# Kernel tuning notes

Hardware: AMD Instinct MI355X
Metric: run time of the kernel (lower is better)

## Reference

```python
import jax, jax.numpy as jnp
import numpy as np

NUM_CLASSES = 2
OVERLAP_THRESHOLD = 0.35
NEG_POS_RATIO = 7
VARIANCES = (0.1, 0.2)
B, P, G = 16, 131072, 32


def point_form(pri):
    # center form (cx,cy,w,h) -> corner form (x1,y1,x2,y2)
    return jnp.concatenate([pri[:, :2] - pri[:, 2:] / 2,
                            pri[:, :2] + pri[:, 2:] / 2], axis=1)


def jaccard(box_a, box_b):
    # box_a [G,4], box_b [P,4], corner form -> IoU [G,P]
    max_xy = jnp.minimum(box_a[:, None, 2:], box_b[None, :, 2:])
    min_xy = jnp.maximum(box_a[:, None, :2], box_b[None, :, :2])
    inter = jnp.prod(jnp.clip(max_xy - min_xy, 0.0, None), axis=2)
    area_a = jnp.prod(box_a[:, 2:] - box_a[:, :2], axis=1)[:, None]
    area_b = jnp.prod(box_b[:, 2:] - box_b[:, :2], axis=1)[None, :]
    return inter / (area_a + area_b - inter)


def encode(matched, pri, variances):
    g_cxcy = ((matched[:, :2] + matched[:, 2:]) / 2 - pri[:, :2]) / (variances[0] * pri[:, 2:])
    g_wh = jnp.log((matched[:, 2:] - matched[:, :2]) / pri[:, 2:]) / variances[1]
    return jnp.concatenate([g_cxcy, g_wh], axis=1)


def encode_landm(matched, pri, variances):
    m = matched.reshape(-1, 5, 2)  # [P,5,2]
    g = (m - pri[:, None, :2]) / (variances[0] * pri[:, None, 2:])
    return g.reshape(-1, 10)


def match_one(truths, landms, labels, pri):
    overlaps = jaccard(truths, point_form(pri))          # [G,P]
    best_prior_idx = jnp.argmax(overlaps, axis=1)        # [G] best prior per gt
    best_truth_overlap = jnp.max(overlaps, axis=0)       # [P]
    best_truth_idx = jnp.argmax(overlaps, axis=0)        # [P]
    # ensure each gt keeps its best prior
    best_truth_overlap = best_truth_overlap.at[best_prior_idx].set(2.0)
    best_truth_idx = best_truth_idx.at[best_prior_idx].set(jnp.arange(truths.shape[0]))
    matches = truths[best_truth_idx]                     # [P,4]
    conf = jnp.where(best_truth_overlap < OVERLAP_THRESHOLD, 0, labels[best_truth_idx])
    loc = encode(matches, pri, VARIANCES)
    landm = encode_landm(landms[best_truth_idx], pri, VARIANCES)
    return loc, conf, landm


def smooth_l1(pred, gt):
    d = jnp.abs(pred - gt)
    return jnp.where(d < 1.0, 0.5 * d * d, d - 0.5)


def multibox_loss(conf_data, loc_data, landm_data, priors, targets):
    batch_size, num_priors = loc_data.shape[0], priors.shape[0]
    truths = targets[:, :, :4]
    landms = targets[:, :, 4:14]
    labels = targets[:, :, 14].astype(jnp.int32)
    loc_t, conf_t, landm_t = jax.vmap(lambda t, l, lb: match_one(t, l, lb, priors))(truths, landms, labels)

    pos = conf_t > 0                                      # [B,P]
    num_pos_total = jnp.maximum(pos.sum().astype(loc_data.dtype), 1.0)
    num_pos_per_image = pos.sum(axis=1, keepdims=True)    # [B,1]
    posf = pos.astype(loc_data.dtype)

    loss_box = (smooth_l1(loc_data, loc_t).sum(-1) * posf).sum()
    loss_landm = (smooth_l1(landm_data, landm_t).sum(-1) * posf).sum()

    logp = jax.nn.log_softmax(conf_data, axis=-1)         # [B,P,C]
    ce = -jnp.take_along_axis(logp, jnp.clip(conf_t, 0, None)[..., None], axis=-1)[..., 0]
    loss_c = jnp.where(pos | (conf_t < 0), 0.0, ce)       # zero pos & ignored
    # hard negative mining: rank by descending loss via double argsort
    loss_idx = jnp.argsort(-loss_c, axis=1)
    idx_rank = jnp.argsort(loss_idx, axis=1)
    num_neg = jnp.minimum(NEG_POS_RATIO * num_pos_per_image, num_priors - 1)
    neg = idx_rank < num_neg
    pn = (pos | neg).astype(conf_data.dtype)
    loss_c_final = (ce * pn).sum()
    return (loss_box / num_pos_total, loss_c_final / num_pos_total, loss_landm / num_pos_total)


def setup_inputs() -> dict:
    key = jax.random.key(0)
    k1, k2, k3, k4, k5, k6, k7 = jax.random.split(key, 7)
    conf_data = jax.random.normal(k1, (B, P, NUM_CLASSES), dtype=jnp.float32)
    loc_data = jax.random.normal(k2, (B, P, 4), dtype=jnp.float32)
    landm_data = jax.random.normal(k3, (B, P, 10), dtype=jnp.float32)
    # priors in center form
    pc = jax.random.uniform(k4, (P, 2), minval=0.0, maxval=1.0)
    pwh = jax.random.uniform(k5, (P, 2), minval=0.02, maxval=0.3)
    priors = jnp.concatenate([pc, pwh], axis=1).astype(jnp.float32)
    # targets: [B,G,15] = corner box(4) + landms(10) + label(1)
    c = jax.random.uniform(k6, (B, G, 2), minval=0.2, maxval=0.8)
    s = jax.random.uniform(k7, (B, G, 2), minval=0.05, maxval=0.3)
    box = jnp.concatenate([c - s / 2, c + s / 2], axis=-1)
    lm = jax.random.uniform(jax.random.fold_in(key, 99), (B, G, 10), minval=0.0, maxval=1.0)
    lbl = jnp.ones((B, G, 1), dtype=jnp.float32)
    targets = jnp.concatenate([box, lm, lbl], axis=-1).astype(jnp.float32)
    return {"conf_data": conf_data, "loc_data": loc_data, "landm_data": landm_data,
            "priors": priors, "targets": targets}


def reference(conf_data, loc_data, landm_data, priors, targets):
    return multibox_loss(conf_data, loc_data, landm_data, priors, targets)
```

## Files before the change

### kernel.cpp

```cpp
#include <hip/hip_runtime.h>
#include <math.h>

#define B_ 16
#define P_ 131072
#define G_ 32
constexpr float OVER_THR = 0.35f;
constexpr float VAR0 = 0.1f;
constexpr float VAR1 = 0.2f;
constexpr int NEG_POS = 7;
constexpr int UNR = 8;
constexpr int LOSS_X = P_ / 256;
constexpr int LOSS_BLOCKS = LOSS_X * B_;
constexpr int NBIN13 = 8192;
constexpr int NBIN8 = 256;
constexpr int NBIN11 = 2048;
constexpr int SCAN_BLKS = 16;

__device__ inline float s1(float d) {
    d = fabsf(d);
    return d < 1.f ? 0.5f * d * d : d - 0.5f;
}

__device__ inline unsigned long long shfl_xor_u64(unsigned long long x, int m) {
    unsigned lo = (unsigned)x, hi = (unsigned)(x >> 32);
    lo = __shfl_xor(lo, m);
    hi = __shfl_xor(hi, m);
    return ((unsigned long long)hi << 32) | lo;
}

template <int NB>
__device__ void topk_select(const unsigned* __restrict__ h, unsigned rem,
                            int* out_bin, unsigned* out_rem) {
    constexpr int CHUNK = NB / 256;
    const int tid = threadIdx.x;
    unsigned cnt[CHUNK];
    unsigned csum = 0;
#pragma unroll
    for (int j = 0; j < CHUNK; ++j) { cnt[j] = h[tid * CHUNK + j]; csum += cnt[j]; }
    __shared__ unsigned ss[256];
    ss[tid] = csum;
    __syncthreads();
    for (int off = 1; off < 256; off <<= 1) {
        unsigned other = (tid + off < 256) ? ss[tid + off] : 0u;
        __syncthreads();
        ss[tid] += other;
        __syncthreads();
    }
    unsigned incl = ss[tid];
    unsigned excl = incl - csum;
    if (excl < rem && incl >= rem) {
        unsigned r = rem - excl, cum = 0;
        int selbin = tid * CHUNK;
#pragma unroll
        for (int j = CHUNK - 1; j >= 0; --j) {
            unsigned c = cnt[j];
            if (cum + c >= r) { selbin = tid * CHUNK + j; r = r - cum; break; }
            cum += c;
        }
        *out_bin = selbin;
        *out_rem = r;
    }
}

__global__ __launch_bounds__(256, 3) void k_match(
        const float4* __restrict__ priors4, const float* __restrict__ targets,
        float* __restrict__ bt_ov, unsigned char* __restrict__ bt_idx,
        unsigned long long* __restrict__ pack) {
    const int b = blockIdx.y;
    const int base = blockIdx.x * (256 * UNR);
    const int tid = threadIdx.x;
    __shared__ float tb[G_][5];
    __shared__ unsigned long long red[G_][4];
    if (tid < G_ * 4) {
        int g = tid >> 2, j = tid & 3;
        tb[g][j] = targets[((size_t)b * G_ + g) * 15 + j];
    }
    __syncthreads();
    if (tid < G_) tb[tid][4] = (tb[tid][2] - tb[tid][0]) * (tb[tid][3] - tb[tid][1]);
    __syncthreads();

    float px1[UNR], py1[UNR], px2[UNR], py2[UNR], pap[UNR], best[UNR];
    int bidx[UNR];
#pragma unroll
    for (int j = 0; j < UNR; ++j) {
        float4 pr = priors4[base + j * 256 + tid];
        px1[j] = pr.x - pr.z * 0.5f;  py1[j] = pr.y - pr.w * 0.5f;
        px2[j] = pr.x + pr.z * 0.5f;  py2[j] = pr.y + pr.w * 0.5f;
        pap[j] = pr.z * pr.w;
        best[j] = -1.0f; bidx[j] = 0;
    }
    const int lane = tid & 63, wave = tid >> 6;
#pragma unroll 2
    for (int g = 0; g < G_; ++g) {
        float t0 = tb[g][0], t1 = tb[g][1], t2 = tb[g][2], t3 = tb[g][3], ta = tb[g][4];
        unsigned long long pk = 0ull;
#pragma unroll
        for (int j = 0; j < UNR; ++j) {
            float iw = fminf(t2, px2[j]) - fmaxf(t0, px1[j]);
            float ih = fminf(t3, py2[j]) - fmaxf(t1, py1[j]);
            float inter = fmaxf(iw, 0.f) * fmaxf(ih, 0.f);
            float iou = inter * __builtin_amdgcn_rcpf(ta + pap[j] - inter);
            if (iou > best[j]) { best[j] = iou; bidx[j] = g; }
            unsigned p = (unsigned)(base + j * 256 + tid);
            unsigned long long cand =
                ((unsigned long long)__float_as_uint(iou) << 32) | (unsigned)(~p);
            if (cand > pk) pk = cand;
        }
#pragma unroll
        for (int off = 32; off > 0; off >>= 1) {
            unsigned long long o = shfl_xor_u64(pk, off);
            if (o > pk) pk = o;
        }
        if (lane == 0) red[g][wave] = pk;
    }
    __syncthreads();
    if (tid < G_) {
        unsigned long long m = red[tid][0];
#pragma unroll
        for (int w = 1; w < 4; ++w) if (red[tid][w] > m) m = red[tid][w];
        atomicMax(&pack[b * G_ + tid], m);
    }
#pragma unroll
    for (int j = 0; j < UNR; ++j) {
        int p = base + j * 256 + tid;
        size_t o = (size_t)b * P_ + p;
        bt_ov[o] = best[j];
        bt_idx[o] = (unsigned char)bidx[j];
    }
}

__global__ void k_override(const unsigned long long* __restrict__ pack,
                           float* __restrict__ bt_ov, unsigned char* __restrict__ bt_idx) {
    int b = threadIdx.x;
    if (b >= B_) return;
    for (int g = 0; g < G_; ++g) {
        unsigned long long pk = pack[b * G_ + g];
        unsigned p = ~(unsigned)(pk & 0xFFFFFFFFull);
        if (p < P_) {
            bt_ov[(size_t)b * P_ + p] = 2.0f;
            bt_idx[(size_t)b * P_ + p] = (unsigned char)g;
        }
    }
}

__global__ __launch_bounds__(256) void k_loss(
        const float2* __restrict__ conf2, const float4* __restrict__ loc4,
        const float* __restrict__ landm, const float4* __restrict__ priors4,
        const float* __restrict__ targets,
        const float* __restrict__ bt_ov, const unsigned char* __restrict__ bt_idx,
        float* __restrict__ ce_neg,
        double* __restrict__ pb, double* __restrict__ pl,
        double* __restrict__ pc, int* __restrict__ pn) {
    const int b = blockIdx.y;
    const int p = blockIdx.x * 256 + threadIdx.x;
    const int tid = threadIdx.x;
    __shared__ float tg[G_ * 15];
    for (int i = tid; i < G_ * 15; i += 256) tg[i] = targets[(size_t)b * G_ * 15 + i];
    __syncthreads();

    const size_t gp = (size_t)b * P_ + p;
    float ov = bt_ov[gp];
    int ti = bt_idx[gp];
    const float* t = &tg[ti * 15];
    float label = t[14];
    int conf_t = (ov < OVER_THR) ? 0 : (int)label;
    bool pos = conf_t > 0;
    int cls = conf_t > 0 ? conf_t : 0;

    float2 c2 = conf2[gp];
    float mx = fmaxf(c2.x, c2.y);
    float lse = mx + logf(expf(c2.x - mx) + expf(c2.y - mx));
    float ce = lse - (cls ? c2.y : c2.x);
    ce_neg[gp] = (!pos && conf_t >= 0) ? ce : 0.f;

    float lb = 0.f, ll = 0.f;
    if (pos) {
        float4 pr = priors4[p];
        float vx = VAR0 * pr.z, vy = VAR0 * pr.w;
        float g0 = ((t[0] + t[2]) * 0.5f - pr.x) / vx;
        float g1 = ((t[1] + t[3]) * 0.5f - pr.y) / vy;
        float g2 = logf((t[2] - t[0]) / pr.z) / VAR1;
        float g3 = logf((t[3] - t[1]) / pr.w) / VAR1;
        float4 ld = loc4[gp];
        lb = s1(ld.x - g0) + s1(ld.y - g1) + s1(ld.z - g2) + s1(ld.w - g3);
        const float* lmp = landm + gp * 10;
#pragma unroll
        for (int i = 0; i < 5; ++i) {
            float2 lm = *(const float2*)(lmp + 2 * i);
            ll += s1(lm.x - (t[4 + 2 * i] - pr.x) / vx)
                + s1(lm.y - (t[5 + 2 * i] - pr.y) / vy);
        }
    }
    double vb = lb, vl = ll, vc = pos ? (double)ce : 0.0;
    int vp = pos ? 1 : 0;
#pragma unroll
    for (int off = 32; off > 0; off >>= 1) {
        vb += __shfl_xor(vb, off);
        vl += __shfl_xor(vl, off);
        vc += __shfl_xor(vc, off);
        vp += __shfl_xor(vp, off);
    }
    __shared__ double rb[4], rl[4], rc[4];
    __shared__ int rp[4];
    int lane = tid & 63, wave = tid >> 6;
    if (lane == 0) { rb[wave] = vb; rl[wave] = vl; rc[wave] = vc; rp[wave] = vp; }
    __syncthreads();
    if (tid == 0) {
        double sb = 0, sl = 0, sc = 0; int sp = 0;
        for (int w = 0; w < 4; ++w) { sb += rb[w]; sl += rl[w]; sc += rc[w]; sp += rp[w]; }
        int bi = blockIdx.y * LOSS_X + blockIdx.x;
        pb[bi] = sb; pl[bi] = sl; pc[bi] = sc; pn[bi] = sp;
    }
}

__global__ __launch_bounds__(1024) void k_hist13(
        const float* __restrict__ ce_neg, unsigned* __restrict__ hist) {
    const int b = blockIdx.y;
    const int tid = threadIdx.x;
    __shared__ unsigned h[NBIN13];
    for (int i = tid; i < NBIN13; i += 1024) h[i] = 0;
    __syncthreads();
    const float4* v4 = (const float4*)(ce_neg + (size_t)b * P_);
    const int c4 = P_ / SCAN_BLKS / 4;
    const int s4 = blockIdx.x * c4;
    for (int i = s4 + tid; i < s4 + c4; i += 1024) {
        float4 x = v4[i];
        atomicAdd(&h[__float_as_uint(x.x) >> 19], 1u);
        atomicAdd(&h[__float_as_uint(x.y) >> 19], 1u);
        atomicAdd(&h[__float_as_uint(x.z) >> 19], 1u);
        atomicAdd(&h[__float_as_uint(x.w) >> 19], 1u);
    }
    __syncthreads();
    unsigned* gh = hist + b * NBIN13;
    for (int i = tid; i < NBIN13; i += 1024)
        if (h[i]) atomicAdd(&gh[i], h[i]);
}

__global__ __launch_bounds__(256) void k_sel13(
        const unsigned* __restrict__ hist, const int* __restrict__ pn,
        int* __restrict__ sel, int* __restrict__ remk, int* __restrict__ npos) {
    const int b = blockIdx.x;
    const int tid = threadIdx.x;
    __shared__ int s_np;
    __shared__ int rnp[4];
    int loc = 0;
    for (int i = tid; i < LOSS_X; i += 256) loc += pn[b * LOSS_X + i];
#pragma unroll
    for (int off = 32; off > 0; off >>= 1) loc += __shfl_xor(loc, off);
    int lane = tid & 63, wave = tid >> 6;
    if (lane == 0) rnp[wave] = loc;
    __syncthreads();
    if (tid == 0) { int s = rnp[0] + rnp[1] + rnp[2] + rnp[3]; s_np = s; npos[b] = s; }
    __syncthreads();
    long long k = (long long)NEG_POS * s_np;
    if (k > P_ - 1) k = P_ - 1;
    if (k <= 0) { if (tid == 0) sel[b] = -1; return; }

    __shared__ int s_bin;
    __shared__ unsigned s_rem;
    topk_select<NBIN13>(hist + b * NBIN13, (unsigned)k, &s_bin, &s_rem);
    __syncthreads();
    if (tid == 0) { sel[b] = s_bin; remk[b] = (int)s_rem; }
}

__global__ __launch_bounds__(1024) void k_hist8(
        const float* __restrict__ ce_neg, const int* __restrict__ sel,
        unsigned* __restrict__ hist8) {
    const int b = blockIdx.y;
    const int s13 = sel[b];
    if (s13 < 0) return;
    const int tid = threadIdx.x;
    __shared__ unsigned h[NBIN8];
    if (tid < NBIN8) h[tid] = 0;
    __syncthreads();
    const float4* v4 = (const float4*)(ce_neg + (size_t)b * P_);
    const int c4 = P_ / SCAN_BLKS / 4;
    const int s4 = blockIdx.x * c4;
    for (int i = s4 + tid; i < s4 + c4; i += 1024) {
        float4 x = v4[i];
        unsigned u0 = __float_as_uint(x.x), u1 = __float_as_uint(x.y);
        unsigned u2 = __float_as_uint(x.z), u3 = __float_as_uint(x.w);
        if ((int)(u0 >> 19) == s13) atomicAdd(&h[(u0 >> 11) & 255u], 1u);
        if ((int)(u1 >> 19) == s13) atomicAdd(&h[(u1 >> 11) & 255u], 1u);
        if ((int)(u2 >> 19) == s13) atomicAdd(&h[(u2 >> 11) & 255u], 1u);
        if ((int)(u3 >> 19) == s13) atomicAdd(&h[(u3 >> 11) & 255u], 1u);
    }
    __syncthreads();
    if (tid < NBIN8 && h[tid]) atomicAdd(&hist8[b * NBIN8 + tid], h[tid]);
}

__global__ __launch_bounds__(256) void k_sel8(
        const unsigned* __restrict__ hist8, const int* __restrict__ sel,
        unsigned* __restrict__ pref, int* __restrict__ remk) {
    const int b = blockIdx.x;
    if (sel[b] < 0) return;
    __shared__ int s_bin;
    __shared__ unsigned s_rem;
    topk_select<NBIN8>(hist8 + b * NBIN8, (unsigned)remk[b], &s_bin, &s_rem);
    __syncthreads();
    if (threadIdx.x == 0) {
        pref[b] = ((unsigned)sel[b] << 8) | (unsigned)s_bin;
        remk[b] = (int)s_rem;
    }
}

__global__ __launch_bounds__(1024) void k_hist11(
        const float* __restrict__ ce_neg, const int* __restrict__ sel,
        const unsigned* __restrict__ pref, unsigned* __restrict__ hist11) {
    const int b = blockIdx.y;
    if (sel[b] < 0) return;
    const unsigned pf = pref[b];
    const int tid = threadIdx.x;
    __shared__ unsigned h[NBIN11];
    for (int i = tid; i < NBIN11; i += 1024) h[i] = 0;
    __syncthreads();
    const float4* v4 = (const float4*)(ce_neg + (size_t)b * P_);
    const int c4 = P_ / SCAN_BLKS / 4;
    const int s4 = blockIdx.x * c4;
    for (int i = s4 + tid; i < s4 + c4; i += 1024) {
        float4 x = v4[i];
        unsigned u0 = __float_as_uint(x.x), u1 = __float_as_uint(x.y);
        unsigned u2 = __float_as_uint(x.z), u3 = __float_as_uint(x.w);
        if ((u0 >> 11) == pf) atomicAdd(&h[u0 & 2047u], 1u);
        if ((u1 >> 11) == pf) atomicAdd(&h[u1 & 2047u], 1u);
        if ((u2 >> 11) == pf) atomicAdd(&h[u2 & 2047u], 1u);
        if ((u3 >> 11) == pf) atomicAdd(&h[u3 & 2047u], 1u);
    }
    __syncthreads();
    unsigned* gh = hist11 + b * NBIN11;
    for (int i = tid; i < NBIN11; i += 1024)
        if (h[i]) atomicAdd(&gh[i], h[i]);
}

__global__ __launch_bounds__(256) void k_sel11(
        const unsigned* __restrict__ hist11, const int* __restrict__ sel,
        const unsigned* __restrict__ pref, const int* __restrict__ remk,
        unsigned* __restrict__ thr, double* __restrict__ tot) {
    const int b = blockIdx.x;
    if (sel[b] < 0) { if (threadIdx.x == 0) thr[b] = 0xFFFFFFFFu; return; }
    __shared__ int s_bin;
    __shared__ unsigned s_rem;
    topk_select<NBIN11>(hist11 + b * NBIN11, (unsigned)remk[b], &s_bin, &s_rem);
    __syncthreads();
    if (threadIdx.x == 0) {
        unsigned t = (pref[b] << 11) | (unsigned)s_bin;
        thr[b] = t;
        atomicAdd(&tot[2], (double)s_rem * (double)__uint_as_float(t));
    }
}

__global__ __launch_bounds__(1024) void k_sumtop(
        const float* __restrict__ ce_neg, const unsigned* __restrict__ thr,
        double* __restrict__ tot) {
    const int b = blockIdx.y;
    const unsigned t = thr[b];
    if (t == 0xFFFFFFFFu) return;
    const int tid = threadIdx.x;
    const float4* v4 = (const float4*)(ce_neg + (size_t)b * P_);
    const int c4 = P_ / SCAN_BLKS / 4;
    const int s4 = blockIdx.x * c4;
    double loc = 0;
    for (int i = s4 + tid; i < s4 + c4; i += 1024) {
        float4 x = v4[i];
        if (__float_as_uint(x.x) > t) loc += x.x;
        if (__float_as_uint(x.y) > t) loc += x.y;
        if (__float_as_uint(x.z) > t) loc += x.z;
        if (__float_as_uint(x.w) > t) loc += x.w;
    }
#pragma unroll
    for (int off = 32; off > 0; off >>= 1) loc += __shfl_xor(loc, off);
    __shared__ double rs[16];
    int lane = tid & 63, wave = tid >> 6;
    if (lane == 0) rs[wave] = loc;
    __syncthreads();
    if (tid == 0) {
        double s = 0;
        for (int w = 0; w < 16; ++w) s += rs[w];
        atomicAdd(&tot[2], s);
    }
}

__global__ __launch_bounds__(1024) void k_final(
        const double* __restrict__ pb, const double* __restrict__ pl,
        const double* __restrict__ pc, const int* __restrict__ npos,
        const double* __restrict__ tot, float* __restrict__ out) {
    int tid = threadIdx.x;
    double sb = 0, sl = 0, sc = 0;
    for (int i = tid; i < LOSS_BLOCKS; i += 1024) {
        sb += pb[i]; sl += pl[i]; sc += pc[i];
    }
#pragma unroll
    for (int off = 32; off > 0; off >>= 1) {
        sb += __shfl_xor(sb, off);
        sl += __shfl_xor(sl, off);
        sc += __shfl_xor(sc, off);
    }
    __shared__ double rb[16], rl[16], rc[16];
    int lane = tid & 63, wave = tid >> 6;
    if (lane == 0) { rb[wave] = sb; rl[wave] = sl; rc[wave] = sc; }
    __syncthreads();
    if (tid == 0) {
        double b2 = 0, l2 = 0, c2 = 0;
        for (int w = 0; w < 16; ++w) { b2 += rb[w]; l2 += rl[w]; c2 += rc[w]; }
        long long tp = 0;
        for (int b = 0; b < B_; ++b) tp += npos[b];
        double n = tp > 0 ? (double)tp : 1.0;
        out[0] = (float)(b2 / n);
        out[1] = (float)((c2 + tot[2]) / n);
        out[2] = (float)(l2 / n);
    }
}

extern "C" void kernel_launch(void* const* d_in, const int* in_sizes, int n_in,
                              void* d_out, int out_size, void* d_ws, size_t ws_size,
                              hipStream_t stream) {
    const float* conf    = (const float*)d_in[0];
    const float* loc     = (const float*)d_in[1];
    const float* landm   = (const float*)d_in[2];
    const float* priors  = (const float*)d_in[3];
    const float* targets = (const float*)d_in[4];

    char* ws = (char*)d_ws;
    double* tot = (double*)ws;
    int* npos = (int*)(ws + 64);
    int* sel  = (int*)(ws + 128);
    int* remk = (int*)(ws + 192);
    unsigned* pref = (unsigned*)(ws + 256);
    unsigned* thr  = (unsigned*)(ws + 320);
    unsigned long long* pack = (unsigned long long*)(ws + 512);
    unsigned* hist13 = (unsigned*)(ws + 4608);
    unsigned* hist8  = hist13 + (size_t)B_ * NBIN13;
    unsigned* hist11 = hist8 + (size_t)B_ * NBIN8;
    size_t zero_bytes = 4608 + (size_t)B_ * (NBIN13 + NBIN8 + NBIN11) * 4;
    size_t big = (zero_bytes + 255) & ~(size_t)255;
    size_t BP = (size_t)B_ * P_;
    float* bt_ov = (float*)(ws + big);
    unsigned char* bt_idx = (unsigned char*)(ws + big + BP * 4);
    float* ce_neg = (float*)(ws + big + BP * 5);
    char* part = ws + big + BP * 9;
    double* pb = (double*)part;
    double* pl = (double*)(part + LOSS_BLOCKS * 8);
    double* pc = (double*)(part + LOSS_BLOCKS * 16);
    int*    pn = (int*)(part + LOSS_BLOCKS * 24);

    hipMemsetAsync(ws, 0, zero_bytes, stream);
    k_match<<<dim3(P_ / (256 * UNR), B_), 256, 0, stream>>>(
        (const float4*)priors, targets, bt_ov, bt_idx, pack);
    k_override<<<1, 64, 0, stream>>>(pack, bt_ov, bt_idx);
    k_loss<<<dim3(LOSS_X, B_), 256, 0, stream>>>(
        (const float2*)conf, (const float4*)loc, landm, (const float4*)priors,
        targets, bt_ov, bt_idx, ce_neg, pb, pl, pc, pn);
    k_hist13<<<dim3(SCAN_BLKS, B_), 1024, 0, stream>>>(ce_neg, hist13);
    k_sel13<<<B_, 256, 0, stream>>>(hist13, pn, sel, remk, npos);
    k_hist8<<<dim3(SCAN_BLKS, B_), 1024, 0, stream>>>(ce_neg, sel, hist8);
    k_sel8<<<B_, 256, 0, stream>>>(hist8, sel, pref, remk);
    k_hist11<<<dim3(SCAN_BLKS, B_), 1024, 0, stream>>>(ce_neg, sel, pref, hist11);
    k_sel11<<<B_, 256, 0, stream>>>(hist11, sel, pref, remk, thr, tot);
    k_sumtop<<<dim3(SCAN_BLKS, B_), 1024, 0, stream>>>(ce_neg, thr, tot);
    k_final<<<1, 1024, 0, stream>>>(pb, pl, pc, npos, tot, (float*)d_out);
}
```

Before: 128.5 us.

## Fuse radix-select passes with per-bin sums and last-block selection, drop override kernel

Restructures the hard-negative top-k. Each radix pass now builds count and sum histograms together, and the last block to finish (found with an atomic ticket) does the bin selection. This cuts the 7 select/hist kernels plus the final sum-above-threshold pass down to 3 scan kernels. The best-prior override is folded into k_loss as a per-thread compare against the 32 packed indices, k_match drops to UNR=4 with an in-thread argmax plus ds_swizzle reductions, and npos is accumulated with atomics. Float atomic sums in shared and global memory make the result order-dependent and add LDS atomic traffic in every pass.

```diff
diff --git a/kernel.cpp b/kernel.cpp
--- a/kernel.cpp
+++ b/kernel.cpp
@@ -8,12 +8,12 @@
 constexpr float VAR0 = 0.1f;
 constexpr float VAR1 = 0.2f;
 constexpr int NEG_POS = 7;
-constexpr int UNR = 8;
+constexpr int UNR = 4;
 constexpr int LOSS_X = P_ / 256;
 constexpr int LOSS_BLOCKS = LOSS_X * B_;
-constexpr int NBIN13 = 8192;
-constexpr int NBIN8 = 256;
-constexpr int NBIN11 = 2048;
+constexpr int NB1 = 4096;
+constexpr int NB2 = 256;
+constexpr int NB3 = 4096;
 constexpr int SCAN_BLKS = 16;
 
 __device__ inline float s1(float d) {
@@ -28,38 +28,64 @@
     return ((unsigned long long)hi << 32) | lo;
 }
 
+template <int IMM>
+__device__ inline unsigned long long swz64(unsigned long long x) {
+    unsigned lo = (unsigned)__builtin_amdgcn_ds_swizzle((int)(unsigned)x, IMM);
+    unsigned hi = (unsigned)__builtin_amdgcn_ds_swizzle((int)(unsigned)(x >> 32), IMM);
+    return ((unsigned long long)hi << 32) | lo;
+}
+
 template <int NB>
-__device__ void topk_select(const unsigned* __restrict__ h, unsigned rem,
-                            int* out_bin, unsigned* out_rem) {
-    constexpr int CHUNK = NB / 256;
+__device__ void blk_select(const unsigned* __restrict__ gc, unsigned rem,
+                           int* sbin, unsigned* srem) {
+    constexpr int CHUNK = (NB + 1023) / 1024;
     const int tid = threadIdx.x;
     unsigned cnt[CHUNK];
     unsigned csum = 0;
 #pragma unroll
-    for (int j = 0; j < CHUNK; ++j) { cnt[j] = h[tid * CHUNK + j]; csum += cnt[j]; }
-    __shared__ unsigned ss[256];
+    for (int j = 0; j < CHUNK; ++j) {
+        int idx = tid * CHUNK + j;
+        unsigned c = (idx < NB) ? gc[idx] : 0u;
+        cnt[j] = c; csum += c;
+    }
+    __shared__ unsigned ss[1024];
     ss[tid] = csum;
     __syncthreads();
-    for (int off = 1; off < 256; off <<= 1) {
-        unsigned other = (tid + off < 256) ? ss[tid + off] : 0u;
+    for (int off = 1; off < 1024; off <<= 1) {
+        unsigned o = (tid + off < 1024) ? ss[tid + off] : 0u;
         __syncthreads();
-        ss[tid] += other;
+        ss[tid] += o;
         __syncthreads();
     }
-    unsigned incl = ss[tid];
-    unsigned excl = incl - csum;
+    unsigned incl = ss[tid], excl = incl - csum;
     if (excl < rem && incl >= rem) {
         unsigned r = rem - excl, cum = 0;
-        int selbin = tid * CHUNK;
+        int sb_ = tid * CHUNK;
 #pragma unroll
         for (int j = CHUNK - 1; j >= 0; --j) {
             unsigned c = cnt[j];
-            if (cum + c >= r) { selbin = tid * CHUNK + j; r = r - cum; break; }
+            if (cum + c >= r) { sb_ = tid * CHUNK + j; r -= cum; break; }
             cum += c;
         }
-        *out_bin = selbin;
-        *out_rem = r;
-    }
+        *sbin = sb_; *srem = r;
+    }
+    __syncthreads();
+}
+
+template <int NB>
+__device__ double blk_sum_above(const float* __restrict__ gs, int bin) {
+    const int tid = threadIdx.x;
+    double a = 0;
+    for (int i = bin + 1 + tid; i < NB; i += 1024) a += (double)gs[i];
+#pragma unroll
+    for (int off = 32; off > 0; off >>= 1) a += __shfl_xor(a, off);
+    __shared__ double rs[16];
+    int lane = tid & 63, wave = tid >> 6;
+    if (lane == 0) rs[wave] = a;
+    __syncthreads();
+    double t = 0;
+    if (tid == 0) for (int w = 0; w < 16; ++w) t += rs[w];
+    return t;
 }
 
 __global__ __launch_bounds__(256, 3) void k_match(
@@ -69,14 +95,15 @@
     const int b = blockIdx.y;
     const int base = blockIdx.x * (256 * UNR);
     const int tid = threadIdx.x;
-    __shared__ float tb[G_][5];
+    __shared__ float4 tb4[G_];
+    __shared__ float tA[G_];
     __shared__ unsigned long long red[G_][4];
-    if (tid < G_ * 4) {
-        int g = tid >> 2, j = tid & 3;
-        tb[g][j] = targets[((size_t)b * G_ + g) * 15 + j];
-    }
-    __syncthreads();
-    if (tid < G_) tb[tid][4] = (tb[tid][2] - tb[tid][0]) * (tb[tid][3] - tb[tid][1]);
+    if (tid < G_) {
+        const float* tp = targets + ((size_t)b * G_ + tid) * 15;
+        float x1 = tp[0], y1 = tp[1], x2 = tp[2], y2 = tp[3];
+        tb4[tid] = make_float4(x1, y1, x2, y2);
+        tA[tid] = (x2 - x1) * (y2 - y1);
+    }
     __syncthreads();
 
     float px1[UNR], py1[UNR], px2[UNR], py2[UNR], pap[UNR], best[UNR];
@@ -92,25 +119,28 @@
     const int lane = tid & 63, wave = tid >> 6;
 #pragma unroll 2
     for (int g = 0; g < G_; ++g) {
-        float t0 = tb[g][0], t1 = tb[g][1], t2 = tb[g][2], t3 = tb[g][3], ta = tb[g][4];
-        unsigned long long pk = 0ull;
+        float4 t = tb4[g];
+        float ta = tA[g];
+        float gb = -1.0f; int gj = 0;
 #pragma unroll
         for (int j = 0; j < UNR; ++j) {
-            float iw = fminf(t2, px2[j]) - fmaxf(t0, px1[j]);
-            float ih = fminf(t3, py2[j]) - fmaxf(t1, py1[j]);
+            float iw = fminf(t.z, px2[j]) - fmaxf(t.x, px1[j]);
+            float ih = fminf(t.w, py2[j]) - fmaxf(t.y, py1[j]);
             float inter = fmaxf(iw, 0.f) * fmaxf(ih, 0.f);
             float iou = inter * __builtin_amdgcn_rcpf(ta + pap[j] - inter);
             if (iou > best[j]) { best[j] = iou; bidx[j] = g; }
-            unsigned p = (unsigned)(base + j * 256 + tid);
-            unsigned long long cand =
-                ((unsigned long long)__float_as_uint(iou) << 32) | (unsigned)(~p);
-            if (cand > pk) pk = cand;
+            if (iou > gb) { gb = iou; gj = j; }
         }
-#pragma unroll
-        for (int off = 32; off > 0; off >>= 1) {
-            unsigned long long o = shfl_xor_u64(pk, off);
-            if (o > pk) pk = o;
-        }
+        unsigned p = (unsigned)(base + (gj << 8) + tid);
+        unsigned long long pk =
+            ((unsigned long long)__float_as_uint(gb) << 32) | (unsigned)(~p);
+        unsigned long long o;
+        o = shfl_xor_u64(pk, 32);  if (o > pk) pk = o;
+        o = swz64<0x401F>(pk);     if (o > pk) pk = o;
+        o = swz64<0x201F>(pk);     if (o > pk) pk = o;
+        o = swz64<0x101F>(pk);     if (o > pk) pk = o;
+        o = swz64<0x081F>(pk);     if (o > pk) pk = o;
+        o = swz64<0x041F>(pk);     if (o > pk) pk = o;
         if (lane == 0) red[g][wave] = pk;
     }
     __syncthreads();
@@ -129,38 +159,29 @@
     }
 }
 
-__global__ void k_override(const unsigned long long* __restrict__ pack,
-                           float* __restrict__ bt_ov, unsigned char* __restrict__ bt_idx) {
-    int b = threadIdx.x;
-    if (b >= B_) return;
-    for (int g = 0; g < G_; ++g) {
-        unsigned long long pk = pack[b * G_ + g];
-        unsigned p = ~(unsigned)(pk & 0xFFFFFFFFull);
-        if (p < P_) {
-            bt_ov[(size_t)b * P_ + p] = 2.0f;
-            bt_idx[(size_t)b * P_ + p] = (unsigned char)g;
-        }
-    }
-}
-
 __global__ __launch_bounds__(256) void k_loss(
         const float2* __restrict__ conf2, const float4* __restrict__ loc4,
         const float* __restrict__ landm, const float4* __restrict__ priors4,
-        const float* __restrict__ targets,
+        const float* __restrict__ targets, const unsigned long long* __restrict__ pack,
         const float* __restrict__ bt_ov, const unsigned char* __restrict__ bt_idx,
         float* __restrict__ ce_neg,
         double* __restrict__ pb, double* __restrict__ pl,
-        double* __restrict__ pc, int* __restrict__ pn) {
+        double* __restrict__ pc, int* __restrict__ npos) {
     const int b = blockIdx.y;
     const int p = blockIdx.x * 256 + threadIdx.x;
     const int tid = threadIdx.x;
     __shared__ float tg[G_ * 15];
+    __shared__ unsigned ptg[G_];
     for (int i = tid; i < G_ * 15; i += 256) tg[i] = targets[(size_t)b * G_ * 15 + i];
+    if (tid < G_) ptg[tid] = ~(unsigned)(pack[b * G_ + tid] & 0xFFFFFFFFull);
     __syncthreads();
 
     const size_t gp = (size_t)b * P_ + p;
     float ov = bt_ov[gp];
     int ti = bt_idx[gp];
+#pragma unroll
+    for (int g = 0; g < G_; ++g)
+        if ((unsigned)p == ptg[g]) { ov = 2.0f; ti = g; }
     const float* t = &tg[ti * 15];
     float label = t[14];
     int conf_t = (ov < OVER_THR) ? 0 : (int)label;
@@ -209,69 +230,22 @@
         double sb = 0, sl = 0, sc = 0; int sp = 0;
         for (int w = 0; w < 4; ++w) { sb += rb[w]; sl += rl[w]; sc += rc[w]; sp += rp[w]; }
         int bi = blockIdx.y * LOSS_X + blockIdx.x;
-        pb[bi] = sb; pl[bi] = sl; pc[bi] = sc; pn[bi] = sp;
-    }
-}
-
-__global__ __launch_bounds__(1024) void k_hist13(
-        const float* __restrict__ ce_neg, unsigned* __restrict__ hist) {
+        pb[bi] = sb; pl[bi] = sl; pc[bi] = sc;
+        if (sp) atomicAdd(&npos[b], sp);
+    }
+}
+
+__global__ __launch_bounds__(1024) void k_ms1(
+        const float* __restrict__ ce_neg, const double* __restrict__ pb,
+        const double* __restrict__ pl, const double* __restrict__ pc,
+        const int* __restrict__ npos, unsigned* __restrict__ gcnt,
+        float* __restrict__ gsum, int* __restrict__ sel, unsigned* __restrict__ remk,
+        int* __restrict__ tick, double* __restrict__ imgsum, double* __restrict__ tot) {
     const int b = blockIdx.y;
     const int tid = threadIdx.x;
-    __shared__ unsigned h[NBIN13];
-    for (int i = tid; i < NBIN13; i += 1024) h[i] = 0;
-    __syncthreads();
-    const float4* v4 = (const float4*)(ce_neg + (size_t)b * P_);
-    const int c4 = P_ / SCAN_BLKS / 4;
-    const int s4 = blockIdx.x * c4;
-    for (int i = s4 + tid; i < s4 + c4; i += 1024) {
-        float4 x = v4[i];
-        atomicAdd(&h[__float_as_uint(x.x) >> 19], 1u);
-        atomicAdd(&h[__float_as_uint(x.y) >> 19], 1u);
-        atomicAdd(&h[__float_as_uint(x.z) >> 19], 1u);
-        atomicAdd(&h[__float_as_uint(x.w) >> 19], 1u);
-    }
-    __syncthreads();
-    unsigned* gh = hist + b * NBIN13;
-    for (int i = tid; i < NBIN13; i += 1024)
-        if (h[i]) atomicAdd(&gh[i], h[i]);
-}
-
-__global__ __launch_bounds__(256) void k_sel13(
-        const unsigned* __restrict__ hist, const int* __restrict__ pn,
-        int* __restrict__ sel, int* __restrict__ remk, int* __restrict__ npos) {
-    const int b = blockIdx.x;
-    const int tid = threadIdx.x;
-    __shared__ int s_np;
-    __shared__ int rnp[4];
-    int loc = 0;
-    for (int i = tid; i < LOSS_X; i += 256) loc += pn[b * LOSS_X + i];
-#pragma unroll
-    for (int off = 32; off > 0; off >>= 1) loc += __shfl_xor(loc, off);
-    int lane = tid & 63, wave = tid >> 6;
-    if (lane == 0) rnp[wave] = loc;
-    __syncthreads();
-    if (tid == 0) { int s = rnp[0] + rnp[1] + rnp[2] + rnp[3]; s_np = s; npos[b] = s; }
-    __syncthreads();
-    long long k = (long long)NEG_POS * s_np;
-    if (k > P_ - 1) k = P_ - 1;
-    if (k <= 0) { if (tid == 0) sel[b] = -1; return; }
-
-    __shared__ int s_bin;
-    __shared__ unsigned s_rem;
-    topk_select<NBIN13>(hist + b * NBIN13, (unsigned)k, &s_bin, &s_rem);
-    __syncthreads();
-    if (tid == 0) { sel[b] = s_bin; remk[b] = (int)s_rem; }
-}
-
-__global__ __launch_bounds__(1024) void k_hist8(
-        const float* __restrict__ ce_neg, const int* __restrict__ sel,
-        unsigned* __restrict__ hist8) {
-    const int b = blockIdx.y;
-    const int s13 = sel[b];
-    if (s13 < 0) return;
-    const int tid = threadIdx.x;
-    __shared__ unsigned h[NBIN8];
-    if (tid < NBIN8) h[tid] = 0;
+    __shared__ unsigned hc[NB1];
+    __shared__ float hs[NB1];
+    for (int i = tid; i < NB1; i += 1024) { hc[i] = 0; hs[i] = 0.f; }
     __syncthreads();
     const float4* v4 = (const float4*)(ce_neg + (size_t)b * P_);
     const int c4 = P_ / SCAN_BLKS / 4;
@@ -280,39 +254,64 @@
         float4 x = v4[i];
         unsigned u0 = __float_as_uint(x.x), u1 = __float_as_uint(x.y);
         unsigned u2 = __float_as_uint(x.z), u3 = __float_as_uint(x.w);
-        if ((int)(u0 >> 19) == s13) atomicAdd(&h[(u0 >> 11) & 255u], 1u);
-        if ((int)(u1 >> 19) == s13) atomicAdd(&h[(u1 >> 11) & 255u], 1u);
-        if ((int)(u2 >> 19) == s13) atomicAdd(&h[(u2 >> 11) & 255u], 1u);
-        if ((int)(u3 >> 19) == s13) atomicAdd(&h[(u3 >> 11) & 255u], 1u);
-    }
-    __syncthreads();
-    if (tid < NBIN8 && h[tid]) atomicAdd(&hist8[b * NBIN8 + tid], h[tid]);
-}
-
-__global__ __launch_bounds__(256) void k_sel8(
-        const unsigned* __restrict__ hist8, const int* __restrict__ sel,
-        unsigned* __restrict__ pref, int* __restrict__ remk) {
-    const int b = blockIdx.x;
-    if (sel[b] < 0) return;
-    __shared__ int s_bin;
-    __shared__ unsigned s_rem;
-    topk_select<NBIN8>(hist8 + b * NBIN8, (unsigned)remk[b], &s_bin, &s_rem);
-    __syncthreads();
-    if (threadIdx.x == 0) {
-        pref[b] = ((unsigned)sel[b] << 8) | (unsigned)s_bin;
-        remk[b] = (int)s_rem;
-    }
-}
-
-__global__ __launch_bounds__(1024) void k_hist11(
+        atomicAdd(&hc[u0 >> 20], 1u); atomicAdd(&hs[u0 >> 20], x.x);
+        atomicAdd(&hc[u1 >> 20], 1u); atomicAdd(&hs[u1 >> 20], x.y);
+        atomicAdd(&hc[u2 >> 20], 1u); atomicAdd(&hs[u2 >> 20], x.z);
+        atomicAdd(&hc[u3 >> 20], 1u); atomicAdd(&hs[u3 >> 20], x.w);
+    }
+    __syncthreads();
+    unsigned* gc = gcnt + b * NB1;
+    float* gs = gsum + b * NB1;
+    for (int i = tid; i < NB1; i += 1024)
+        if (hc[i]) { atomicAdd(&gc[i], hc[i]); atomicAdd(&gs[i], hs[i]); }
+    __threadfence();
+    __shared__ int amLast;
+    if (tid == 0) amLast = (atomicAdd(&tick[b], 1) == SCAN_BLKS - 1);
+    __syncthreads();
+    if (!amLast) return;
+    __threadfence();
+    double sb = 0, sl = 0, sc = 0;
+    for (int i = tid; i < LOSS_X; i += 1024) {
+        sb += pb[b * LOSS_X + i]; sl += pl[b * LOSS_X + i]; sc += pc[b * LOSS_X + i];
+    }
+#pragma unroll
+    for (int off = 32; off > 0; off >>= 1) {
+        sb += __shfl_xor(sb, off); sl += __shfl_xor(sl, off); sc += __shfl_xor(sc, off);
+    }
+    __shared__ double r3[16][3];
+    int lane = tid & 63, wave = tid >> 6;
+    if (lane == 0) { r3[wave][0] = sb; r3[wave][1] = sl; r3[wave][2] = sc; }
+    __syncthreads();
+    if (tid == 0) {
+        double a = 0, c = 0, d = 0;
+        for (int w = 0; w < 16; ++w) { a += r3[w][0]; c += r3[w][1]; d += r3[w][2]; }
+        imgsum[b * 3 + 0] = a; imgsum[b * 3 + 1] = c; imgsum[b * 3 + 2] = d;
+    }
+    long long k = (long long)NEG_POS * npos[b];
+    if (k > P_ - 1) k = P_ - 1;
+    if (k <= 0) { if (tid == 0) sel[b] = -1; return; }
+    __shared__ int sb_;
+    __shared__ unsigned sr_;
+    blk_select<NB1>(gc, (unsigned)k, &sb_, &sr_);
+    double above = blk_sum_above<NB1>(gs, sb_);
+    if (tid == 0) {
+        atomicAdd(&tot[2], above);
+        sel[b] = sb_; remk[b] = sr_;
+    }
+}
+
+__global__ __launch_bounds__(1024) void k_ms2(
         const float* __restrict__ ce_neg, const int* __restrict__ sel,
-        const unsigned* __restrict__ pref, unsigned* __restrict__ hist11) {
+        unsigned* __restrict__ gcnt, float* __restrict__ gsum,
+        unsigned* __restrict__ pref, unsigned* __restrict__ remk,
+        int* __restrict__ tick, double* __restrict__ tot) {
     const int b = blockIdx.y;
-    if (sel[b] < 0) return;
-    const unsigned pf = pref[b];
-    const int tid = threadIdx.x;
-    __shared__ unsigned h[NBIN11];
-    for (int i = tid; i < NBIN11; i += 1024) h[i] = 0;
+    const int s1v = sel[b];
+    if (s1v < 0) return;
+    const int tid = threadIdx.x;
+    __shared__ unsigned hc[NB2];
+    __shared__ float hs[NB2];
+    if (tid < NB2) { hc[tid] = 0; hs[tid] = 0.f; }
     __syncthreads();
     const float4* v4 = (const float4*)(ce_neg + (size_t)b * P_);
     const int c4 = P_ / SCAN_BLKS / 4;
@@ -321,93 +320,94 @@
         float4 x = v4[i];
         unsigned u0 = __float_as_uint(x.x), u1 = __float_as_uint(x.y);
         unsigned u2 = __float_as_uint(x.z), u3 = __float_as_uint(x.w);
-        if ((u0 >> 11) == pf) atomicAdd(&h[u0 & 2047u], 1u);
-        if ((u1 >> 11) == pf) atomicAdd(&h[u1 & 2047u], 1u);
-        if ((u2 >> 11) == pf) atomicAdd(&h[u2 & 2047u], 1u);
-        if ((u3 >> 11) == pf) atomicAdd(&h[u3 & 2047u], 1u);
-    }
-    __syncthreads();
-    unsigned* gh = hist11 + b * NBIN11;
-    for (int i = tid; i < NBIN11; i += 1024)
-        if (h[i]) atomicAdd(&gh[i], h[i]);
-}
-
-__global__ __launch_bounds__(256) void k_sel11(
-        const unsigned* __restrict__ hist11, const int* __restrict__ sel,
-        const unsigned* __restrict__ pref, const int* __restrict__ remk,
-        unsigned* __restrict__ thr, double* __restrict__ tot) {
-    const int b = blockIdx.x;
-    if (sel[b] < 0) { if (threadIdx.x == 0) thr[b] = 0xFFFFFFFFu; return; }
-    __shared__ int s_bin;
-    __shared__ unsigned s_rem;
-    topk_select<NBIN11>(hist11 + b * NBIN11, (unsigned)remk[b], &s_bin, &s_rem);
-    __syncthreads();
-    if (threadIdx.x == 0) {
-        unsigned t = (pref[b] << 11) | (unsigned)s_bin;
-        thr[b] = t;
-        atomicAdd(&tot[2], (double)s_rem * (double)__uint_as_float(t));
-    }
-}
-
-__global__ __launch_bounds__(1024) void k_sumtop(
-        const float* __restrict__ ce_neg, const unsigned* __restrict__ thr,
-        double* __restrict__ tot) {
+        if ((int)(u0 >> 20) == s1v) { atomicAdd(&hc[(u0 >> 12) & 255u], 1u); atomicAdd(&hs[(u0 >> 12) & 255u], x.x); }
+        if ((int)(u1 >> 20) == s1v) { atomicAdd(&hc[(u1 >> 12) & 255u], 1u); atomicAdd(&hs[(u1 >> 12) & 255u], x.y); }
+        if ((int)(u2 >> 20) == s1v) { atomicAdd(&hc[(u2 >> 12) & 255u], 1u); atomicAdd(&hs[(u2 >> 12) & 255u], x.z); }
+        if ((int)(u3 >> 20) == s1v) { atomicAdd(&hc[(u3 >> 12) & 255u], 1u); atomicAdd(&hs[(u3 >> 12) & 255u], x.w); }
+    }
+    __syncthreads();
+    unsigned* gc = gcnt + b * NB2;
+    float* gs = gsum + b * NB2;
+    if (tid < NB2 && hc[tid]) { atomicAdd(&gc[tid], hc[tid]); atomicAdd(&gs[tid], hs[tid]); }
+    __threadfence();
+    __shared__ int amLast;
+    if (tid == 0) amLast = (atomicAdd(&tick[b], 1) == SCAN_BLKS - 1);
+    __syncthreads();
+    if (!amLast) return;
+    __threadfence();
+    __shared__ int sb_;
+    __shared__ unsigned sr_;
+    blk_select<NB2>(gc, remk[b], &sb_, &sr_);
+    double above = blk_sum_above<NB2>(gs, sb_);
+    if (tid == 0) {
+        atomicAdd(&tot[2], above);
+        pref[b] = ((unsigned)s1v << 8) | (unsigned)sb_;
+        remk[b] = sr_;
+    }
+}
+
+__global__ __launch_bounds__(1024) void k_ms3(
+        const float* __restrict__ ce_neg, const int* __restrict__ sel,
+        const unsigned* __restrict__ pref, const unsigned* __restrict__ remk,
+        unsigned* __restrict__ gcnt, float* __restrict__ gsum,
+        int* __restrict__ tick, double* __restrict__ tot) {
     const int b = blockIdx.y;
-    const unsigned t = thr[b];
-    if (t == 0xFFFFFFFFu) return;
-    const int tid = threadIdx.x;
+    if (sel[b] < 0) return;
+    const unsigned pf = pref[b];
+    const int tid = threadIdx.x;
+    __shared__ unsigned hc[NB3];
+    __shared__ float hs[NB3];
+    for (int i = tid; i < NB3; i += 1024) { hc[i] = 0; hs[i] = 0.f; }
+    __syncthreads();
     const float4* v4 = (const float4*)(ce_neg + (size_t)b * P_);
     const int c4 = P_ / SCAN_BLKS / 4;
     const int s4 = blockIdx.x * c4;
-    double loc = 0;
     for (int i = s4 + tid; i < s4 + c4; i += 1024) {
         float4 x = v4[i];
-        if (__float_as_uint(x.x) > t) loc += x.x;
-        if (__float_as_uint(x.y) > t) loc += x.y;
-        if (__float_as_uint(x.z) > t) loc += x.z;
-        if (__float_as_uint(x.w) > t) loc += x.w;
-    }
-#pragma unroll
-    for (int off = 32; off > 0; off >>= 1) loc += __shfl_xor(loc, off);
-    __shared__ double rs[16];
-    int lane = tid & 63, wave = tid >> 6;
-    if (lane == 0) rs[wave] = loc;
-    __syncthreads();
+        unsigned u0 = __float_as_uint(x.x), u1 = __float_as_uint(x.y);
+        unsigned u2 = __float_as_uint(x.z), u3 = __float_as_uint(x.w);
+        if ((u0 >> 12) == pf) { atomicAdd(&hc[u0 & 4095u], 1u); atomicAdd(&hs[u0 & 4095u], x.x); }
+        if ((u1 >> 12) == pf) { atomicAdd(&hc[u1 & 4095u], 1u); atomicAdd(&hs[u1 & 4095u], x.y); }
+        if ((u2 >> 12) == pf) { atomicAdd(&hc[u2 & 4095u], 1u); atomicAdd(&hs[u2 & 4095u], x.z); }
+        if ((u3 >> 12) == pf) { atomicAdd(&hc[u3 & 4095u], 1u); atomicAdd(&hs[u3 & 4095u], x.w); }
+    }
+    __syncthreads();
+    unsigned* gc = gcnt + b * NB3;
+    float* gs = gsum + b * NB3;
+    for (int i = tid; i < NB3; i += 1024)
+        if (hc[i]) { atomicAdd(&gc[i], hc[i]); atomicAdd(&gs[i], hs[i]); }
+    __threadfence();
+    __shared__ int amLast;
+    if (tid == 0) amLast = (atomicAdd(&tick[b], 1) == SCAN_BLKS - 1);
+    __syncthreads();
+    if (!amLast) return;
+    __threadfence();
+    __shared__ int sb_;
+    __shared__ unsigned sr_;
+    blk_select<NB3>(gc, remk[b], &sb_, &sr_);
+    double above = blk_sum_above<NB3>(gs, sb_);
     if (tid == 0) {
-        double s = 0;
-        for (int w = 0; w < 16; ++w) s += rs[w];
-        atomicAdd(&tot[2], s);
-    }
-}
-
-__global__ __launch_bounds__(1024) void k_final(
-        const double* __restrict__ pb, const double* __restrict__ pl,
-        const double* __restrict__ pc, const int* __restrict__ npos,
-        const double* __restrict__ tot, float* __restrict__ out) {
-    int tid = threadIdx.x;
-    double sb = 0, sl = 0, sc = 0;
-    for (int i = tid; i < LOSS_BLOCKS; i += 1024) {
-        sb += pb[i]; sl += pl[i]; sc += pc[i];
-    }
-#pragma unroll
-    for (int off = 32; off > 0; off >>= 1) {
-        sb += __shfl_xor(sb, off);
-        sl += __shfl_xor(sl, off);
-        sc += __shfl_xor(sc, off);
-    }
-    __shared__ double rb[16], rl[16], rc[16];
-    int lane = tid & 63, wave = tid >> 6;
-    if (lane == 0) { rb[wave] = sb; rl[wave] = sl; rc[wave] = sc; }
-    __syncthreads();
-    if (tid == 0) {
-        double b2 = 0, l2 = 0, c2 = 0;
-        for (int w = 0; w < 16; ++w) { b2 += rb[w]; l2 += rl[w]; c2 += rc[w]; }
+        unsigned T = (pf << 12) | (unsigned)sb_;
+        atomicAdd(&tot[2], above + (double)sr_ * (double)__uint_as_float(T));
+    }
+}
+
+__global__ void k_final(const double* __restrict__ imgsum,
+                        const int* __restrict__ npos,
+                        const double* __restrict__ tot, float* __restrict__ out) {
+    if (threadIdx.x == 0) {
+        double sb = 0, sl = 0, sc = 0;
         long long tp = 0;
-        for (int b = 0; b < B_; ++b) tp += npos[b];
+        for (int b = 0; b < B_; ++b) {
+            sb += imgsum[b * 3 + 0];
+            sl += imgsum[b * 3 + 1];
+            sc += imgsum[b * 3 + 2];
+            tp += npos[b];
+        }
         double n = tp > 0 ? (double)tp : 1.0;
-        out[0] = (float)(b2 / n);
-        out[1] = (float)((c2 + tot[2]) / n);
-        out[2] = (float)(l2 / n);
+        out[0] = (float)(sb / n);
+        out[1] = (float)((sc + tot[2]) / n);
+        out[2] = (float)(sl / n);
     }
 }
 
@@ -424,14 +424,20 @@
     double* tot = (double*)ws;
     int* npos = (int*)(ws + 64);
     int* sel  = (int*)(ws + 128);
-    int* remk = (int*)(ws + 192);
+    unsigned* remk = (unsigned*)(ws + 192);
     unsigned* pref = (unsigned*)(ws + 256);
-    unsigned* thr  = (unsigned*)(ws + 320);
+    int* tick1 = (int*)(ws + 320);
+    int* tick2 = (int*)(ws + 384);
+    int* tick3 = (int*)(ws + 448);
     unsigned long long* pack = (unsigned long long*)(ws + 512);
-    unsigned* hist13 = (unsigned*)(ws + 4608);
-    unsigned* hist8  = hist13 + (size_t)B_ * NBIN13;
-    unsigned* hist11 = hist8 + (size_t)B_ * NBIN8;
-    size_t zero_bytes = 4608 + (size_t)B_ * (NBIN13 + NBIN8 + NBIN11) * 4;
+    double* imgsum = (double*)(ws + 4608);
+    unsigned* gcnt1 = (unsigned*)(ws + 5120);
+    float*    gsum1 = (float*)((char*)gcnt1 + (size_t)B_ * NB1 * 4);
+    unsigned* gcnt2 = (unsigned*)((char*)gsum1 + (size_t)B_ * NB1 * 4);
+    float*    gsum2 = (float*)((char*)gcnt2 + (size_t)B_ * NB2 * 4);
+    unsigned* gcnt3 = (unsigned*)((char*)gsum2 + (size_t)B_ * NB2 * 4);
+    float*    gsum3 = (float*)((char*)gcnt3 + (size_t)B_ * NB3 * 4);
+    size_t zero_bytes = 5120 + (size_t)B_ * (NB1 * 2 + NB2 * 2 + NB3 * 2) * 4;
     size_t big = (zero_bytes + 255) & ~(size_t)255;
     size_t BP = (size_t)B_ * P_;
     float* bt_ov = (float*)(ws + big);
@@ -441,21 +447,18 @@
     double* pb = (double*)part;
     double* pl = (double*)(part + LOSS_BLOCKS * 8);
     double* pc = (double*)(part + LOSS_BLOCKS * 16);
-    int*    pn = (int*)(part + LOSS_BLOCKS * 24);
 
     hipMemsetAsync(ws, 0, zero_bytes, stream);
     k_match<<<dim3(P_ / (256 * UNR), B_), 256, 0, stream>>>(
         (const float4*)priors, targets, bt_ov, bt_idx, pack);
-    k_override<<<1, 64, 0, stream>>>(pack, bt_ov, bt_idx);
     k_loss<<<dim3(LOSS_X, B_), 256, 0, stream>>>(
         (const float2*)conf, (const float4*)loc, landm, (const float4*)priors,
-        targets, bt_ov, bt_idx, ce_neg, pb, pl, pc, pn);
-    k_hist13<<<dim3(SCAN_BLKS, B_), 1024, 0, stream>>>(ce_neg, hist13);
-    k_sel13<<<B_, 256, 0, stream>>>(hist13, pn, sel, remk, npos);
-    k_hist8<<<dim3(SCAN_BLKS, B_), 1024, 0, stream>>>(ce_neg, sel, hist8);
-    k_sel8<<<B_, 256, 0, stream>>>(hist8, sel, pref, remk);
-    k_hist11<<<dim3(SCAN_BLKS, B_), 1024, 0, stream>>>(ce_neg, sel, pref, hist11);
-    k_sel11<<<B_, 256, 0, stream>>>(hist11, sel, pref, remk, thr, tot);
-    k_sumtop<<<dim3(SCAN_BLKS, B_), 1024, 0, stream>>>(ce_neg, thr, tot);
-    k_final<<<1, 1024, 0, stream>>>(pb, pl, pc, npos, tot, (float*)d_out);
-}
+        targets, pack, bt_ov, bt_idx, ce_neg, pb, pl, pc, npos);
+    k_ms1<<<dim3(SCAN_BLKS, B_), 1024, 0, stream>>>(
+        ce_neg, pb, pl, pc, npos, gcnt1, gsum1, sel, remk, tick1, imgsum, tot);
+    k_ms2<<<dim3(SCAN_BLKS, B_), 1024, 0, stream>>>(
+        ce_neg, sel, gcnt2, gsum2, pref, remk, tick2, tot);
+    k_ms3<<<dim3(SCAN_BLKS, B_), 1024, 0, stream>>>(
+        ce_neg, sel, pref, remk, gcnt3, gsum3, tick3, tot);
+    k_final<<<1, 64, 0, stream>>>(imgsum, npos, tot, (float*)d_out);
+}
```

Result: slower. 405.7 us (+215.7%).
